# Performance work log

Measured on AMD Instinct MI355X. Metric: run time of the kernel, lower is better.

Reference implementation:

```python
import jax, jax.numpy as jnp
import numpy as np

N, E, H, P, B = 50000, 800000, 128, 8, 512


def setup_inputs() -> dict:
    key = jax.random.key(0)
    ks = jax.random.split(key, 10)
    return {
        "node_attrs": jax.random.normal(ks[0], (N, P - 1, H), jnp.float32),
        "edge_attrs": jax.random.normal(ks[1], (E, H), jnp.float32),
        "instruction": jax.random.normal(ks[2], (H,), jnp.float32),
        "prop_embeds": jax.random.normal(ks[3], (P, H), jnp.float32),
        "distribution": jax.random.uniform(ks[4], (N,), jnp.float32),
        "Ws_property": jax.random.uniform(ks[5], (P, H, H), jnp.float32),
        "W_state": jax.random.uniform(ks[6], (H,), jnp.float32),
        "W_relation": jax.random.uniform(ks[7], (H,), jnp.float32),
        "edge_indices": jax.random.randint(ks[8], (2, E), 0, N),
        "node_graph": jnp.sort(jax.random.randint(ks[9], (N,), 0, B)),
        "num_graphs": B,
    }


def _segment_softmax(logits, seg, num_segments):
    # per-graph softmax over nodes (equiv. of torch.sparse.softmax(dim=1))
    m = jax.ops.segment_max(logits, seg, num_segments=num_segments)
    e = jnp.exp(logits - m[seg])
    s = jax.ops.segment_sum(e, seg, num_segments=num_segments)
    return e / s[seg]


def reference(node_attrs, edge_attrs, instruction, prop_embeds, distribution,
              Ws_property, W_state, W_relation, edge_indices, node_graph,
              num_graphs):
    # property similarities: softmax over P
    prop_sim = jax.nn.softmax(prop_embeds @ instruction)  # [P]
    # per-property projection of node attributes: [N, P-1, H]
    node_proj = jnp.einsum('phk,npk->nph', Ws_property[:-1], node_attrs)
    # weighted sum over properties, gated by instruction: [N, H]
    node_scores = jax.nn.elu(
        jnp.einsum('p,h,nph->nh', prop_sim[:-1], instruction, node_proj))
    # relation-property projection of edge attributes: [E, H]
    edge_scores = jax.nn.elu(instruction * (edge_attrs @ Ws_property[-1].T))
    # state path logits: [N]
    state_logits = node_scores @ W_state
    # relation path: scatter-add messages to edge targets, weighted by source distribution
    src, dst = edge_indices[0], edge_indices[1]
    agg = jnp.zeros_like(node_scores).at[dst].add(
        distribution[src, None] * edge_scores)  # [N, H]
    rel_logits = agg @ W_relation  # [N]
    p_rel = prop_sim[-1]
    next_dist = (p_rel * _segment_softmax(rel_logits, node_graph, num_graphs)
                 + (1.0 - p_rel) * _segment_softmax(state_logits, node_graph, num_graphs))
    return next_dist
```

## Files before the change

kernel.cpp:

```cpp
#include <hip/hip_runtime.h>
#include <math.h>

#define H_DIM 128
#define NPROP 8
#define NGRAPHS 512
#define LDS_STRIDE 136

typedef short short8 __attribute__((ext_vector_type(8)));
typedef float f32x4 __attribute__((ext_vector_type(4)));
typedef unsigned short ushort_t;

__device__ __forceinline__ void split_bf16(float x, ushort_t& hb, ushort_t& lb) {
  unsigned u = __float_as_uint(x);
  hb = (ushort_t)(u >> 16);
  float hf = __uint_as_float(u & 0xFFFF0000u);
  float lf = x - hf;
  unsigned ul = __float_as_uint(lf);
  lb = (ushort_t)((ul + 0x8000u) >> 16);
}

__device__ __forceinline__ void split8(const float4 u, const float4 v,
                                       short8& h, short8& l) {
  ushort_t* hp = (ushort_t*)&h;
  ushort_t* lp = (ushort_t*)&l;
  split_bf16(u.x, hp[0], lp[0]);
  split_bf16(u.y, hp[1], lp[1]);
  split_bf16(u.z, hp[2], lp[2]);
  split_bf16(u.w, hp[3], lp[3]);
  split_bf16(v.x, hp[4], lp[4]);
  split_bf16(v.y, hp[5], lp[5]);
  split_bf16(v.z, hp[6], lp[6]);
  split_bf16(v.w, hp[7], lp[7]);
}

__device__ __forceinline__ float elu_f(float y) {
  return y > 0.f ? y : (__expf(y) - 1.f);
}

__global__ void prep_prop_sim(const float* __restrict__ prop_embeds,
                              const float* __restrict__ instruction,
                              float* __restrict__ prop_sim) {
  __shared__ float dots[NPROP];
  int wave = threadIdx.x >> 6;
  int lane = threadIdx.x & 63;
  float v = prop_embeds[wave * H_DIM + lane] * instruction[lane] +
            prop_embeds[wave * H_DIM + 64 + lane] * instruction[64 + lane];
#pragma unroll
  for (int off = 32; off > 0; off >>= 1) v += __shfl_down(v, off);
  if (lane == 0) dots[wave] = v;
  __syncthreads();
  if (threadIdx.x == 0) {
    float m = dots[0];
    for (int p = 1; p < NPROP; ++p) m = fmaxf(m, dots[p]);
    float e[NPROP], s = 0.f;
    for (int p = 0; p < NPROP; ++p) { e[p] = expf(dots[p] - m); s += e[p]; }
    for (int p = 0; p < NPROP; ++p) prop_sim[p] = e[p] / s;
  }
}

__global__ void prep_weights(const float* __restrict__ Ws,
                             const float* __restrict__ instruction,
                             const float* __restrict__ prop_sim,
                             ushort_t* __restrict__ Wh,
                             ushort_t* __restrict__ Wl) {
  int idx = blockIdx.x * 256 + threadIdx.x;
  int p = idx >> 14;
  int h = (idx >> 7) & 127;
  float s = (p < 7) ? prop_sim[p] : 1.0f;
  float w = s * instruction[h] * Ws[idx];
  ushort_t hb, lb;
  split_bf16(w, hb, lb);
  Wh[idx] = hb;
  Wl[idx] = lb;
}

__global__ void __launch_bounds__(256) fused_mfma_kernel(
    const float* __restrict__ node_attrs,
    const float* __restrict__ edge_attrs,
    const ushort_t* __restrict__ Wh,
    const ushort_t* __restrict__ Wl,
    const float* __restrict__ W_state,
    const float* __restrict__ W_relation,
    const float* __restrict__ distribution,
    const int* __restrict__ src_idx,
    const int* __restrict__ dst_idx,
    float* __restrict__ state_logits,
    float* __restrict__ rel_logits,
    int N, int nodeBlocks) {
  __shared__ __align__(16) ushort_t Ah[128 * LDS_STRIDE];
  __shared__ __align__(16) ushort_t Al[128 * LDS_STRIDE];
  const int t = threadIdx.x;
  const int lane = t & 63;
  const int wave = t >> 6;
  const int col = lane & 15;
  const int quad = lane >> 4;
  const int r0 = wave * 32 + col;
  const int kq = quad * 8;

  f32x4 acc[8][2];
#pragma unroll
  for (int m = 0; m < 8; ++m) {
    acc[m][0] = (f32x4){0.f, 0.f, 0.f, 0.f};
    acc[m][1] = (f32x4){0.f, 0.f, 0.f, 0.f};
  }

  if (blockIdx.x >= nodeBlocks) {
    const long tile = (long)(blockIdx.x - nodeBlocks) * 128;
    const float* X0 = edge_attrs + (tile + r0) * H_DIM;
    const float* X1 = X0 + 16 * H_DIM;

    float4 ca0 = *(const float4*)(X0 + kq);
    float4 ca1 = *(const float4*)(X0 + kq + 4);
    float4 cb0 = *(const float4*)(X1 + kq);
    float4 cb1 = *(const float4*)(X1 + kq + 4);

    {
      const ushort_t* Wp_h = Wh + 7 * (H_DIM * H_DIM);
      const ushort_t* Wp_l = Wl + 7 * (H_DIM * H_DIM);
#pragma unroll
      for (int i = 0; i < 8; ++i) {
        int f = i * 256 + t;
        int row = f >> 4;
        int c8 = (f & 15) * 8;
        *(short8*)&Ah[row * LDS_STRIDE + c8] = *(const short8*)&Wp_h[row * H_DIM + c8];
        *(short8*)&Al[row * LDS_STRIDE + c8] = *(const short8*)&Wp_l[row * H_DIM + c8];
      }
    }
    __syncthreads();

#pragma unroll
    for (int ks = 0; ks < 4; ++ks) {
      float4 na0 = ca0, na1 = ca1, nb0 = cb0, nb1 = cb1;
      if (ks < 3) {
        int ko = (ks + 1) * 32 + kq;
        na0 = *(const float4*)(X0 + ko);
        na1 = *(const float4*)(X0 + ko + 4);
        nb0 = *(const float4*)(X1 + ko);
        nb1 = *(const float4*)(X1 + ko + 4);
      }
      short8 b0h, b0l, b1h, b1l;
      split8(ca0, ca1, b0h, b0l);
      split8(cb0, cb1, b1h, b1l);
      const int kk = ks * 32 + kq;
#pragma unroll
      for (int m = 0; m < 8; ++m) {
        const int wi = (m * 16 + col) * LDS_STRIDE + kk;
        short8 ah = *(const short8*)&Ah[wi];
        short8 al = *(const short8*)&Al[wi];
        acc[m][0] = __builtin_amdgcn_mfma_f32_16x16x32_bf16(ah, b0h, acc[m][0], 0, 0, 0);
        acc[m][0] = __builtin_amdgcn_mfma_f32_16x16x32_bf16(ah, b0l, acc[m][0], 0, 0, 0);
        acc[m][0] = __builtin_amdgcn_mfma_f32_16x16x32_bf16(al, b0h, acc[m][0], 0, 0, 0);
        acc[m][1] = __builtin_amdgcn_mfma_f32_16x16x32_bf16(ah, b1h, acc[m][1], 0, 0, 0);
        acc[m][1] = __builtin_amdgcn_mfma_f32_16x16x32_bf16(ah, b1l, acc[m][1], 0, 0, 0);
        acc[m][1] = __builtin_amdgcn_mfma_f32_16x16x32_bf16(al, b1h, acc[m][1], 0, 0, 0);
      }
      ca0 = na0; ca1 = na1; cb0 = nb0; cb1 = nb1;
    }

    float s0 = 0.f, s1 = 0.f;
#pragma unroll
    for (int m = 0; m < 8; ++m) {
      float4 wv = *(const float4*)(W_relation + m * 16 + quad * 4);
      s0 += wv.x * elu_f(acc[m][0][0]) + wv.y * elu_f(acc[m][0][1]) +
            wv.z * elu_f(acc[m][0][2]) + wv.w * elu_f(acc[m][0][3]);
      s1 += wv.x * elu_f(acc[m][1][0]) + wv.y * elu_f(acc[m][1][1]) +
            wv.z * elu_f(acc[m][1][2]) + wv.w * elu_f(acc[m][1][3]);
    }
    s0 += __shfl_xor(s0, 16); s0 += __shfl_xor(s0, 32);
    s1 += __shfl_xor(s1, 16); s1 += __shfl_xor(s1, 32);
    if (lane < 32) {
      long e = tile + wave * 32 + lane;
      float sv = (lane & 16) ? s1 : s0;
      int s = src_idx[e], d = dst_idx[e];
      atomicAdd(rel_logits + d, distribution[s] * sv);
    }
  } else {
    const long tile = (long)blockIdx.x * 128;
    const long n0 = tile + r0;
    const long n1 = n0 + 16;
    const bool v0 = n0 < N;
    const bool v1 = n1 < N;
    const float* B0 = node_attrs + n0 * (7 * H_DIM);
    const float* B1 = node_attrs + n1 * (7 * H_DIM);
    const float4 z4 = make_float4(0.f, 0.f, 0.f, 0.f);

    float4 ca0 = z4, ca1 = z4, cb0 = z4, cb1 = z4;
    if (v0) { ca0 = *(const float4*)(B0 + kq); ca1 = *(const float4*)(B0 + kq + 4); }
    if (v1) { cb0 = *(const float4*)(B1 + kq); cb1 = *(const float4*)(B1 + kq + 4); }

    for (int p = 0; p < 7; ++p) {
      __syncthreads();
      {
        const ushort_t* Wp_h = Wh + p * (H_DIM * H_DIM);
        const ushort_t* Wp_l = Wl + p * (H_DIM * H_DIM);
#pragma unroll
        for (int i = 0; i < 8; ++i) {
          int f = i * 256 + t;
          int row = f >> 4;
          int c8 = (f & 15) * 8;
          *(short8*)&Ah[row * LDS_STRIDE + c8] = *(const short8*)&Wp_h[row * H_DIM + c8];
          *(short8*)&Al[row * LDS_STRIDE + c8] = *(const short8*)&Wp_l[row * H_DIM + c8];
        }
      }
      __syncthreads();

#pragma unroll
      for (int ks = 0; ks < 4; ++ks) {
        float4 na0 = z4, na1 = z4, nb0 = z4, nb1 = z4;
        int np = p, nks = ks + 1;
        if (nks == 4) { np = p + 1; nks = 0; }
        if (np < 7) {
          int off = np * H_DIM + nks * 32 + kq;
          if (v0) { na0 = *(const float4*)(B0 + off); na1 = *(const float4*)(B0 + off + 4); }
          if (v1) { nb0 = *(const float4*)(B1 + off); nb1 = *(const float4*)(B1 + off + 4); }
        }
        short8 b0h, b0l, b1h, b1l;
        split8(ca0, ca1, b0h, b0l);
        split8(cb0, cb1, b1h, b1l);
        const int kk = ks * 32 + kq;
#pragma unroll
        for (int m = 0; m < 8; ++m) {
          const int wi = (m * 16 + col) * LDS_STRIDE + kk;
          short8 ah = *(const short8*)&Ah[wi];
          short8 al = *(const short8*)&Al[wi];
          acc[m][0] = __builtin_amdgcn_mfma_f32_16x16x32_bf16(ah, b0h, acc[m][0], 0, 0, 0);
          acc[m][0] = __builtin_amdgcn_mfma_f32_16x16x32_bf16(ah, b0l, acc[m][0], 0, 0, 0);
          acc[m][0] = __builtin_amdgcn_mfma_f32_16x16x32_bf16(al, b0h, acc[m][0], 0, 0, 0);
          acc[m][1] = __builtin_amdgcn_mfma_f32_16x16x32_bf16(ah, b1h, acc[m][1], 0, 0, 0);
          acc[m][1] = __builtin_amdgcn_mfma_f32_16x16x32_bf16(ah, b1l, acc[m][1], 0, 0, 0);
          acc[m][1] = __builtin_amdgcn_mfma_f32_16x16x32_bf16(al, b1h, acc[m][1], 0, 0, 0);
        }
        ca0 = na0; ca1 = na1; cb0 = nb0; cb1 = nb1;
      }
    }

    float s0 = 0.f, s1 = 0.f;
#pragma unroll
    for (int m = 0; m < 8; ++m) {
      float4 wv = *(const float4*)(W_state + m * 16 + quad * 4);
      s0 += wv.x * elu_f(acc[m][0][0]) + wv.y * elu_f(acc[m][0][1]) +
            wv.z * elu_f(acc[m][0][2]) + wv.w * elu_f(acc[m][0][3]);
      s1 += wv.x * elu_f(acc[m][1][0]) + wv.y * elu_f(acc[m][1][1]) +
            wv.z * elu_f(acc[m][1][2]) + wv.w * elu_f(acc[m][1][3]);
    }
    s0 += __shfl_xor(s0, 16); s0 += __shfl_xor(s0, 32);
    s1 += __shfl_xor(s1, 16); s1 += __shfl_xor(s1, 32);
    if (lane < 32) {
      long n = tile + wave * 32 + lane;
      if (n < N) state_logits[n] = (lane & 16) ? s1 : s0;
    }
  }
}

__device__ __forceinline__ float wave_red_max(float v) {
#pragma unroll
  for (int off = 32; off > 0; off >>= 1) v = fmaxf(v, __shfl_down(v, off));
  return v;
}
__device__ __forceinline__ float wave_red_sum(float v) {
#pragma unroll
  for (int off = 32; off > 0; off >>= 1) v += __shfl_down(v, off);
  return v;
}

__global__ void finalize_kernel(const float* __restrict__ state_logits,
                                const float* __restrict__ rel_logits,
                                const int* __restrict__ node_graph,
                                const float* __restrict__ prop_sim,
                                float* __restrict__ out, int N) {
  int g = blockIdx.x;
  __shared__ int bounds[2];
  if (threadIdx.x == 0) {
    int a = 0, b = N;
    while (a < b) { int m = (a + b) >> 1; if (node_graph[m] < g) a = m + 1; else b = m; }
    bounds[0] = a;
    b = N;
    while (a < b) { int m = (a + b) >> 1; if (node_graph[m] < g + 1) a = m + 1; else b = m; }
    bounds[1] = a;
  }
  __syncthreads();
  int lo = bounds[0], hi = bounds[1];
  if (lo >= hi) return;

  int lane = threadIdx.x & 63, w = threadIdx.x >> 6;
  __shared__ float redS[4], redR[4];

  float mS = -3.0e38f, mR = -3.0e38f;
  for (int i = lo + threadIdx.x; i < hi; i += blockDim.x) {
    mS = fmaxf(mS, state_logits[i]);
    mR = fmaxf(mR, rel_logits[i]);
  }
  mS = wave_red_max(mS); mR = wave_red_max(mR);
  if (lane == 0) { redS[w] = mS; redR[w] = mR; }
  __syncthreads();
  mS = fmaxf(fmaxf(redS[0], redS[1]), fmaxf(redS[2], redS[3]));
  mR = fmaxf(fmaxf(redR[0], redR[1]), fmaxf(redR[2], redR[3]));
  __syncthreads();

  float sS = 0.f, sR = 0.f;
  for (int i = lo + threadIdx.x; i < hi; i += blockDim.x) {
    sS += expf(state_logits[i] - mS);
    sR += expf(rel_logits[i] - mR);
  }
  sS = wave_red_sum(sS); sR = wave_red_sum(sR);
  if (lane == 0) { redS[w] = sS; redR[w] = sR; }
  __syncthreads();
  sS = redS[0] + redS[1] + redS[2] + redS[3];
  sR = redR[0] + redR[1] + redR[2] + redR[3];

  float p_rel = prop_sim[NPROP - 1];
  float invS = 1.0f / sS, invR = 1.0f / sR;
  for (int i = lo + threadIdx.x; i < hi; i += blockDim.x) {
    float ps = expf(state_logits[i] - mS) * invS;
    float pr = expf(rel_logits[i] - mR) * invR;
    out[i] = p_rel * pr + (1.0f - p_rel) * ps;
  }
}

extern "C" void kernel_launch(void* const* d_in, const int* in_sizes, int n_in,
                              void* d_out, int out_size, void* d_ws, size_t ws_size,
                              hipStream_t stream) {
  const float* node_attrs   = (const float*)d_in[0];
  const float* edge_attrs   = (const float*)d_in[1];
  const float* instruction  = (const float*)d_in[2];
  const float* prop_embeds  = (const float*)d_in[3];
  const float* distribution = (const float*)d_in[4];
  const float* Ws_property  = (const float*)d_in[5];
  const float* W_state      = (const float*)d_in[6];
  const float* W_relation   = (const float*)d_in[7];
  const int*   edge_indices = (const int*)d_in[8];
  const int*   node_graph   = (const int*)d_in[9];

  int N = in_sizes[4];
  int E = in_sizes[1] / H_DIM;
  float* out = (float*)d_out;

  char* w = (char*)d_ws;
  size_t nBytes = ((size_t)N * 4 + 15) & ~(size_t)15;
  float*    prop_sim     = (float*)w;
  float*    state_logits = (float*)(w + 256);
  float*    rel_logits   = (float*)(w + 256 + nBytes);
  ushort_t* Wh           = (ushort_t*)(w + 256 + 2 * nBytes);
  ushort_t* Wl           = Wh + NPROP * H_DIM * H_DIM;

  hipMemsetAsync(rel_logits, 0, (size_t)N * 4, stream);

  prep_prop_sim<<<1, 512, 0, stream>>>(prop_embeds, instruction, prop_sim);
  prep_weights<<<NPROP * H_DIM * H_DIM / 256, 256, 0, stream>>>(
      Ws_property, instruction, prop_sim, Wh, Wl);

  int nodeBlocks = (N + 127) / 128;
  int edgeBlocks = E / 128;
  fused_mfma_kernel<<<nodeBlocks + edgeBlocks, 256, 0, stream>>>(
      node_attrs, edge_attrs, Wh, Wl, W_state, W_relation,
      distribution, edge_indices, edge_indices + E,
      state_logits, rel_logits, N, nodeBlocks);

  finalize_kernel<<<NGRAPHS, 256, 0, stream>>>(state_logits, rel_logits,
                                               node_graph, prop_sim, out, N);
}
```

Before: 727.9 us.

## Persistent 1024-block grid with cost-weighted edge/node tile split and fused prep

Replaces the one-tile-per-block grid with 1024 persistent blocks that each take a contiguous range of work units, where a node tile counts as seven edge tiles. Edge blocks load the relation weight into LDS once and loop over many tiles, double-buffering edge rows across tile boundaries. The prop_sim softmax and the rel_logits zeroing are folded into prep_weights, which removes one launch and a memset. In exchange, node tiles reload all seven weight matrices per tile, and a block whose range straddles both kinds pays both setup costs.

Result: slower. 772.0 us (+6.1%).

```diff
diff --git a/kernel.cpp b/kernel.cpp
--- a/kernel.cpp
+++ b/kernel.cpp
@@ -5,6 +5,7 @@
 #define NPROP 8
 #define NGRAPHS 512
 #define LDS_STRIDE 136
+#define W_NODE 7
 
 typedef short short8 __attribute__((ext_vector_type(8)));
 typedef float f32x4 __attribute__((ext_vector_type(4)));
@@ -37,41 +38,44 @@
   return y > 0.f ? y : (__expf(y) - 1.f);
 }
 
-__global__ void prep_prop_sim(const float* __restrict__ prop_embeds,
-                              const float* __restrict__ instruction,
-                              float* __restrict__ prop_sim) {
-  __shared__ float dots[NPROP];
-  int wave = threadIdx.x >> 6;
-  int lane = threadIdx.x & 63;
-  float v = prop_embeds[wave * H_DIM + lane] * instruction[lane] +
-            prop_embeds[wave * H_DIM + 64 + lane] * instruction[64 + lane];
-#pragma unroll
-  for (int off = 32; off > 0; off >>= 1) v += __shfl_down(v, off);
-  if (lane == 0) dots[wave] = v;
-  __syncthreads();
-  if (threadIdx.x == 0) {
-    float m = dots[0];
-    for (int p = 1; p < NPROP; ++p) m = fmaxf(m, dots[p]);
-    float e[NPROP], s = 0.f;
-    for (int p = 0; p < NPROP; ++p) { e[p] = expf(dots[p] - m); s += e[p]; }
-    for (int p = 0; p < NPROP; ++p) prop_sim[p] = e[p] / s;
-  }
-}
-
 __global__ void prep_weights(const float* __restrict__ Ws,
                              const float* __restrict__ instruction,
-                             const float* __restrict__ prop_sim,
+                             const float* __restrict__ prop_embeds,
                              ushort_t* __restrict__ Wh,
-                             ushort_t* __restrict__ Wl) {
-  int idx = blockIdx.x * 256 + threadIdx.x;
-  int p = idx >> 14;
-  int h = (idx >> 7) & 127;
-  float s = (p < 7) ? prop_sim[p] : 1.0f;
-  float w = s * instruction[h] * Ws[idx];
+                             ushort_t* __restrict__ Wl,
+                             float* __restrict__ prop_sim,
+                             float* __restrict__ rel_logits, int N) {
+  __shared__ float dots[NPROP];
+  const int t = threadIdx.x;
+  const int wave = t >> 6;
+  const int lane = t & 63;
+  for (int pp = wave; pp < NPROP; pp += 4) {
+    float v = prop_embeds[pp * H_DIM + lane] * instruction[lane] +
+              prop_embeds[pp * H_DIM + 64 + lane] * instruction[64 + lane];
+#pragma unroll
+    for (int off = 32; off > 0; off >>= 1) v += __shfl_down(v, off);
+    if (lane == 0) dots[pp] = v;
+  }
+  __syncthreads();
+  float m = dots[0];
+#pragma unroll
+  for (int p = 1; p < NPROP; ++p) m = fmaxf(m, dots[p]);
+  float ex[NPROP], s = 0.f;
+#pragma unroll
+  for (int p = 0; p < NPROP; ++p) { ex[p] = expf(dots[p] - m); s += ex[p]; }
+
+  const int idx = blockIdx.x * 256 + t;
+  const int p = idx >> 14;
+  const int h = (idx >> 7) & 127;
+  float sp = (p < 7) ? ex[p] / s : 1.0f;
+  float w = sp * instruction[h] * Ws[idx];
   ushort_t hb, lb;
   split_bf16(w, hb, lb);
   Wh[idx] = hb;
   Wl[idx] = lb;
+
+  if (blockIdx.x == 0 && t < NPROP) prop_sim[t] = ex[t] / s;
+  for (int i = idx; i < N; i += NPROP * H_DIM * H_DIM) rel_logits[i] = 0.f;
 }
 
 __global__ void __launch_bounds__(256) fused_mfma_kernel(
@@ -86,7 +90,7 @@
     const int* __restrict__ dst_idx,
     float* __restrict__ state_logits,
     float* __restrict__ rel_logits,
-    int N, int nodeBlocks) {
+    int N, int TE, int TN) {
   __shared__ __align__(16) ushort_t Ah[128 * LDS_STRIDE];
   __shared__ __align__(16) ushort_t Al[128 * LDS_STRIDE];
   const int t = threadIdx.x;
@@ -97,22 +101,29 @@
   const int r0 = wave * 32 + col;
   const int kq = quad * 8;
 
-  f32x4 acc[8][2];
-#pragma unroll
-  for (int m = 0; m < 8; ++m) {
-    acc[m][0] = (f32x4){0.f, 0.f, 0.f, 0.f};
-    acc[m][1] = (f32x4){0.f, 0.f, 0.f, 0.f};
-  }
-
-  if (blockIdx.x >= nodeBlocks) {
-    const long tile = (long)(blockIdx.x - nodeBlocks) * 128;
-    const float* X0 = edge_attrs + (tile + r0) * H_DIM;
-    const float* X1 = X0 + 16 * H_DIM;
-
-    float4 ca0 = *(const float4*)(X0 + kq);
-    float4 ca1 = *(const float4*)(X0 + kq + 4);
-    float4 cb0 = *(const float4*)(X1 + kq);
-    float4 cb1 = *(const float4*)(X1 + kq + 4);
+  const int NB = gridDim.x;
+  const long U = (long)TE + (long)TN * W_NODE;
+  const long u0 = (long)blockIdx.x * U / NB;
+  const long u1 = ((long)blockIdx.x + 1) * U / NB;
+  const int e0 = (int)((u0 < TE) ? u0 : TE);
+  const int e1 = (int)((u1 < TE) ? u1 : TE);
+  int n0 = 0, n1 = 0;
+  if (u1 > TE) {
+    n0 = (u0 > TE) ? (int)((u0 - TE + W_NODE - 1) / W_NODE) : 0;
+    n1 = (int)((u1 - TE + W_NODE - 1) / W_NODE);
+    if (n1 > TN) n1 = TN;
+  }
+
+  if (e1 > e0) {
+    const float* P = edge_attrs + ((long)e0 * 128 + r0) * H_DIM;
+    float4 c00 = *(const float4*)(P + kq);
+    float4 c01 = *(const float4*)(P + kq + 4);
+    float4 c10 = *(const float4*)(P + 16 * H_DIM + kq);
+    float4 c11 = *(const float4*)(P + 16 * H_DIM + kq + 4);
+    float4 n00 = *(const float4*)(P + 32 + kq);
+    float4 n01 = *(const float4*)(P + 32 + kq + 4);
+    float4 n10 = *(const float4*)(P + 16 * H_DIM + 32 + kq);
+    float4 n11 = *(const float4*)(P + 16 * H_DIM + 32 + kq + 4);
 
     {
       const ushort_t* Wp_h = Wh + 7 * (H_DIM * H_DIM);
@@ -128,95 +139,34 @@
     }
     __syncthreads();
 
-#pragma unroll
-    for (int ks = 0; ks < 4; ++ks) {
-      float4 na0 = ca0, na1 = ca1, nb0 = cb0, nb1 = cb1;
-      if (ks < 3) {
-        int ko = (ks + 1) * 32 + kq;
-        na0 = *(const float4*)(X0 + ko);
-        na1 = *(const float4*)(X0 + ko + 4);
-        nb0 = *(const float4*)(X1 + ko);
-        nb1 = *(const float4*)(X1 + ko + 4);
-      }
-      short8 b0h, b0l, b1h, b1l;
-      split8(ca0, ca1, b0h, b0l);
-      split8(cb0, cb1, b1h, b1l);
-      const int kk = ks * 32 + kq;
+    float4 wrel[8];
+#pragma unroll
+    for (int m = 0; m < 8; ++m)
+      wrel[m] = *(const float4*)(W_relation + m * 16 + quad * 4);
+
+    for (int tt = e0; tt < e1; ++tt) {
+      const float* Q = edge_attrs + ((long)(tt + 1) * 128 + r0) * H_DIM;
+      f32x4 acc[8][2];
 #pragma unroll
       for (int m = 0; m < 8; ++m) {
-        const int wi = (m * 16 + col) * LDS_STRIDE + kk;
-        short8 ah = *(const short8*)&Ah[wi];
-        short8 al = *(const short8*)&Al[wi];
-        acc[m][0] = __builtin_amdgcn_mfma_f32_16x16x32_bf16(ah, b0h, acc[m][0], 0, 0, 0);
-        acc[m][0] = __builtin_amdgcn_mfma_f32_16x16x32_bf16(ah, b0l, acc[m][0], 0, 0, 0);
-        acc[m][0] = __builtin_amdgcn_mfma_f32_16x16x32_bf16(al, b0h, acc[m][0], 0, 0, 0);
-        acc[m][1] = __builtin_amdgcn_mfma_f32_16x16x32_bf16(ah, b1h, acc[m][1], 0, 0, 0);
-        acc[m][1] = __builtin_amdgcn_mfma_f32_16x16x32_bf16(ah, b1l, acc[m][1], 0, 0, 0);
-        acc[m][1] = __builtin_amdgcn_mfma_f32_16x16x32_bf16(al, b1h, acc[m][1], 0, 0, 0);
-      }
-      ca0 = na0; ca1 = na1; cb0 = nb0; cb1 = nb1;
-    }
-
-    float s0 = 0.f, s1 = 0.f;
-#pragma unroll
-    for (int m = 0; m < 8; ++m) {
-      float4 wv = *(const float4*)(W_relation + m * 16 + quad * 4);
-      s0 += wv.x * elu_f(acc[m][0][0]) + wv.y * elu_f(acc[m][0][1]) +
-            wv.z * elu_f(acc[m][0][2]) + wv.w * elu_f(acc[m][0][3]);
-      s1 += wv.x * elu_f(acc[m][1][0]) + wv.y * elu_f(acc[m][1][1]) +
-            wv.z * elu_f(acc[m][1][2]) + wv.w * elu_f(acc[m][1][3]);
-    }
-    s0 += __shfl_xor(s0, 16); s0 += __shfl_xor(s0, 32);
-    s1 += __shfl_xor(s1, 16); s1 += __shfl_xor(s1, 32);
-    if (lane < 32) {
-      long e = tile + wave * 32 + lane;
-      float sv = (lane & 16) ? s1 : s0;
-      int s = src_idx[e], d = dst_idx[e];
-      atomicAdd(rel_logits + d, distribution[s] * sv);
-    }
-  } else {
-    const long tile = (long)blockIdx.x * 128;
-    const long n0 = tile + r0;
-    const long n1 = n0 + 16;
-    const bool v0 = n0 < N;
-    const bool v1 = n1 < N;
-    const float* B0 = node_attrs + n0 * (7 * H_DIM);
-    const float* B1 = node_attrs + n1 * (7 * H_DIM);
-    const float4 z4 = make_float4(0.f, 0.f, 0.f, 0.f);
-
-    float4 ca0 = z4, ca1 = z4, cb0 = z4, cb1 = z4;
-    if (v0) { ca0 = *(const float4*)(B0 + kq); ca1 = *(const float4*)(B0 + kq + 4); }
-    if (v1) { cb0 = *(const float4*)(B1 + kq); cb1 = *(const float4*)(B1 + kq + 4); }
-
-    for (int p = 0; p < 7; ++p) {
-      __syncthreads();
-      {
-        const ushort_t* Wp_h = Wh + p * (H_DIM * H_DIM);
-        const ushort_t* Wp_l = Wl + p * (H_DIM * H_DIM);
-#pragma unroll
-        for (int i = 0; i < 8; ++i) {
-          int f = i * 256 + t;
-          int row = f >> 4;
-          int c8 = (f & 15) * 8;
-          *(short8*)&Ah[row * LDS_STRIDE + c8] = *(const short8*)&Wp_h[row * H_DIM + c8];
-          *(short8*)&Al[row * LDS_STRIDE + c8] = *(const short8*)&Wp_l[row * H_DIM + c8];
-        }
-      }
-      __syncthreads();
-
+        acc[m][0] = (f32x4){0.f, 0.f, 0.f, 0.f};
+        acc[m][1] = (f32x4){0.f, 0.f, 0.f, 0.f};
+      }
 #pragma unroll
       for (int ks = 0; ks < 4; ++ks) {
-        float4 na0 = z4, na1 = z4, nb0 = z4, nb1 = z4;
-        int np = p, nks = ks + 1;
-        if (nks == 4) { np = p + 1; nks = 0; }
-        if (np < 7) {
-          int off = np * H_DIM + nks * 32 + kq;
-          if (v0) { na0 = *(const float4*)(B0 + off); na1 = *(const float4*)(B0 + off + 4); }
-          if (v1) { nb0 = *(const float4*)(B1 + off); nb1 = *(const float4*)(B1 + off + 4); }
-        }
+        float4 p00, p01, p10, p11;
+        const bool have = (ks < 2) || (tt + 1 < e1);
+        const float* S = (ks < 2) ? (P + (ks + 2) * 32) : (Q + (ks - 2) * 32);
+        if (have) {
+          p00 = *(const float4*)(S + kq);
+          p01 = *(const float4*)(S + kq + 4);
+          p10 = *(const float4*)(S + 16 * H_DIM + kq);
+          p11 = *(const float4*)(S + 16 * H_DIM + kq + 4);
+        } else { p00 = c00; p01 = c01; p10 = c10; p11 = c11; }
+
         short8 b0h, b0l, b1h, b1l;
-        split8(ca0, ca1, b0h, b0l);
-        split8(cb0, cb1, b1h, b1l);
+        split8(c00, c01, b0h, b0l);
+        split8(c10, c11, b1h, b1l);
         const int kk = ks * 32 + kq;
 #pragma unroll
         for (int m = 0; m < 8; ++m) {
@@ -230,24 +180,117 @@
           acc[m][1] = __builtin_amdgcn_mfma_f32_16x16x32_bf16(ah, b1l, acc[m][1], 0, 0, 0);
           acc[m][1] = __builtin_amdgcn_mfma_f32_16x16x32_bf16(al, b1h, acc[m][1], 0, 0, 0);
         }
-        ca0 = na0; ca1 = na1; cb0 = nb0; cb1 = nb1;
-      }
+        c00 = n00; c01 = n01; c10 = n10; c11 = n11;
+        n00 = p00; n01 = p01; n10 = p10; n11 = p11;
+      }
+
+      float s0 = 0.f, s1 = 0.f;
+#pragma unroll
+      for (int m = 0; m < 8; ++m) {
+        s0 += wrel[m].x * elu_f(acc[m][0][0]) + wrel[m].y * elu_f(acc[m][0][1]) +
+              wrel[m].z * elu_f(acc[m][0][2]) + wrel[m].w * elu_f(acc[m][0][3]);
+        s1 += wrel[m].x * elu_f(acc[m][1][0]) + wrel[m].y * elu_f(acc[m][1][1]) +
+              wrel[m].z * elu_f(acc[m][1][2]) + wrel[m].w * elu_f(acc[m][1][3]);
+      }
+      s0 += __shfl_xor(s0, 16); s0 += __shfl_xor(s0, 32);
+      s1 += __shfl_xor(s1, 16); s1 += __shfl_xor(s1, 32);
+      if (lane < 32) {
+        long e = (long)tt * 128 + wave * 32 + lane;
+        float sv = (lane & 16) ? s1 : s0;
+        int s = src_idx[e], d = dst_idx[e];
+        atomicAdd(rel_logits + d, distribution[s] * sv);
+      }
+      P = Q;
     }
-
-    float s0 = 0.f, s1 = 0.f;
-#pragma unroll
-    for (int m = 0; m < 8; ++m) {
-      float4 wv = *(const float4*)(W_state + m * 16 + quad * 4);
-      s0 += wv.x * elu_f(acc[m][0][0]) + wv.y * elu_f(acc[m][0][1]) +
-            wv.z * elu_f(acc[m][0][2]) + wv.w * elu_f(acc[m][0][3]);
-      s1 += wv.x * elu_f(acc[m][1][0]) + wv.y * elu_f(acc[m][1][1]) +
-            wv.z * elu_f(acc[m][1][2]) + wv.w * elu_f(acc[m][1][3]);
-    }
-    s0 += __shfl_xor(s0, 16); s0 += __shfl_xor(s0, 32);
-    s1 += __shfl_xor(s1, 16); s1 += __shfl_xor(s1, 32);
-    if (lane < 32) {
-      long n = tile + wave * 32 + lane;
-      if (n < N) state_logits[n] = (lane & 16) ? s1 : s0;
+  }
+
+  if (n1 > n0) {
+    float4 wst[8];
+#pragma unroll
+    for (int m = 0; m < 8; ++m)
+      wst[m] = *(const float4*)(W_state + m * 16 + quad * 4);
+    const float4 z4 = make_float4(0.f, 0.f, 0.f, 0.f);
+
+    for (int nt = n0; nt < n1; ++nt) {
+      const long tile = (long)nt * 128;
+      const long nd0 = tile + r0;
+      const long nd1 = nd0 + 16;
+      const bool v0 = nd0 < N;
+      const bool v1 = nd1 < N;
+      const float* B0 = node_attrs + nd0 * (7 * H_DIM);
+      const float* B1 = node_attrs + nd1 * (7 * H_DIM);
+
+      f32x4 acc[8][2];
+#pragma unroll
+      for (int m = 0; m < 8; ++m) {
+        acc[m][0] = (f32x4){0.f, 0.f, 0.f, 0.f};
+        acc[m][1] = (f32x4){0.f, 0.f, 0.f, 0.f};
+      }
+
+      float4 ca0 = z4, ca1 = z4, cb0 = z4, cb1 = z4;
+      if (v0) { ca0 = *(const float4*)(B0 + kq); ca1 = *(const float4*)(B0 + kq + 4); }
+      if (v1) { cb0 = *(const float4*)(B1 + kq); cb1 = *(const float4*)(B1 + kq + 4); }
+
+      for (int p = 0; p < 7; ++p) {
+        __syncthreads();
+        {
+          const ushort_t* Wp_h = Wh + p * (H_DIM * H_DIM);
+          const ushort_t* Wp_l = Wl + p * (H_DIM * H_DIM);
+#pragma unroll
+          for (int i = 0; i < 8; ++i) {
+            int f = i * 256 + t;
+            int row = f >> 4;
+            int c8 = (f & 15) * 8;
+            *(short8*)&Ah[row * LDS_STRIDE + c8] = *(const short8*)&Wp_h[row * H_DIM + c8];
+            *(short8*)&Al[row * LDS_STRIDE + c8] = *(const short8*)&Wp_l[row * H_DIM + c8];
+          }
+        }
+        __syncthreads();
+
+#pragma unroll
+        for (int ks = 0; ks < 4; ++ks) {
+          float4 na0 = z4, na1 = z4, nb0 = z4, nb1 = z4;
+          int np = p, nks = ks + 1;
+          if (nks == 4) { np = p + 1; nks = 0; }
+          if (np < 7) {
+            int off = np * H_DIM + nks * 32 + kq;
+            if (v0) { na0 = *(const float4*)(B0 + off); na1 = *(const float4*)(B0 + off + 4); }
+            if (v1) { nb0 = *(const float4*)(B1 + off); nb1 = *(const float4*)(B1 + off + 4); }
+          }
+          short8 b0h, b0l, b1h, b1l;
+          split8(ca0, ca1, b0h, b0l);
+          split8(cb0, cb1, b1h, b1l);
+          const int kk = ks * 32 + kq;
+#pragma unroll
+          for (int m = 0; m < 8; ++m) {
+            const int wi = (m * 16 + col) * LDS_STRIDE + kk;
+            short8 ah = *(const short8*)&Ah[wi];
+            short8 al = *(const short8*)&Al[wi];
+            acc[m][0] = __builtin_amdgcn_mfma_f32_16x16x32_bf16(ah, b0h, acc[m][0], 0, 0, 0);
+            acc[m][0] = __builtin_amdgcn_mfma_f32_16x16x32_bf16(ah, b0l, acc[m][0], 0, 0, 0);
+            acc[m][0] = __builtin_amdgcn_mfma_f32_16x16x32_bf16(al, b0h, acc[m][0], 0, 0, 0);
+            acc[m][1] = __builtin_amdgcn_mfma_f32_16x16x32_bf16(ah, b1h, acc[m][1], 0, 0, 0);
+            acc[m][1] = __builtin_amdgcn_mfma_f32_16x16x32_bf16(ah, b1l, acc[m][1], 0, 0, 0);
+            acc[m][1] = __builtin_amdgcn_mfma_f32_16x16x32_bf16(al, b1h, acc[m][1], 0, 0, 0);
+          }
+          ca0 = na0; ca1 = na1; cb0 = nb0; cb1 = nb1;
+        }
+      }
+
+      float s0 = 0.f, s1 = 0.f;
+#pragma unroll
+      for (int m = 0; m < 8; ++m) {
+        s0 += wst[m].x * elu_f(acc[m][0][0]) + wst[m].y * elu_f(acc[m][0][1]) +
+              wst[m].z * elu_f(acc[m][0][2]) + wst[m].w * elu_f(acc[m][0][3]);
+        s1 += wst[m].x * elu_f(acc[m][1][0]) + wst[m].y * elu_f(acc[m][1][1]) +
+              wst[m].z * elu_f(acc[m][1][2]) + wst[m].w * elu_f(acc[m][1][3]);
+      }
+      s0 += __shfl_xor(s0, 16); s0 += __shfl_xor(s0, 32);
+      s1 += __shfl_xor(s1, 16); s1 += __shfl_xor(s1, 32);
+      if (lane < 32) {
+        long n = tile + wave * 32 + lane;
+        if (n < N) state_logits[n] = (lane & 16) ? s1 : s0;
+      }
     }
   }
 }
@@ -343,18 +386,15 @@
   ushort_t* Wh           = (ushort_t*)(w + 256 + 2 * nBytes);
   ushort_t* Wl           = Wh + NPROP * H_DIM * H_DIM;
 
-  hipMemsetAsync(rel_logits, 0, (size_t)N * 4, stream);
-
-  prep_prop_sim<<<1, 512, 0, stream>>>(prop_embeds, instruction, prop_sim);
   prep_weights<<<NPROP * H_DIM * H_DIM / 256, 256, 0, stream>>>(
-      Ws_property, instruction, prop_sim, Wh, Wl);
-
-  int nodeBlocks = (N + 127) / 128;
-  int edgeBlocks = E / 128;
-  fused_mfma_kernel<<<nodeBlocks + edgeBlocks, 256, 0, stream>>>(
+      Ws_property, instruction, prop_embeds, Wh, Wl, prop_sim, rel_logits, N);
+
+  int TE = E / 128;
+  int TN = (N + 127) / 128;
+  fused_mfma_kernel<<<1024, 256, 0, stream>>>(
       node_attrs, edge_attrs, Wh, Wl, W_state, W_relation,
       distribution, edge_indices, edge_indices + E,
-      state_logits, rel_logits, N, nodeBlocks);
+      state_logits, rel_logits, N, TE, TN);
 
   finalize_kernel<<<NGRAPHS, 256, 0, stream>>>(state_logits, rel_logits,
                                                node_graph, prop_sim, out, N);
```
